# Kernel optimization log

Measured on AMD Instinct MI355X. Metric: run time of the kernel, lower is better.

## Reference

```python
import jax, jax.numpy as jnp
import numpy as np
from jax import lax

WIN_SIZE = 11
SIGMA = 1.5
WEIGHTS = jnp.array([0.0448, 0.2856, 0.3001, 0.2363, 0.1333], dtype=jnp.float32)
C1 = (0.01 * 1.0) ** 2  # val_range = 1.0
C2 = (0.03 * 1.0) ** 2


def gaussian_kernel2d(kernel_size, sigma):
    g = jnp.arange(kernel_size, dtype=jnp.float32) - kernel_size // 2
    g = jnp.exp(-(g ** 2) / (2.0 * sigma ** 2))
    g = g / g.sum()
    return jnp.outer(g, g)  # [k, k]


def depthwise_conv(x, k2d):
    # x: [B, C, H, W]; same gaussian window applied per-channel (groups=C), VALID padding
    C = x.shape[1]
    w = jnp.broadcast_to(k2d, (C, 1) + k2d.shape).astype(x.dtype)
    return lax.conv_general_dilated(x, w, (1, 1), 'VALID',
                                    feature_group_count=C,
                                    dimension_numbers=('NCHW', 'OIHW', 'NCHW'))


def ssim_index(x, y, k2d, nonnegative=True):
    # returns (ss, cs) each of shape [B, C] (spatial mean, per channel)
    m1 = depthwise_conv(x, k2d)
    m2 = depthwise_conv(y, k2d)
    m12 = m1 * m2
    m1s = m1 * m1
    m2s = m2 * m2
    v1 = depthwise_conv(x * x, k2d) - m1s
    v2 = depthwise_conv(y * y, k2d) - m2s
    cov = depthwise_conv(x * y, k2d) - m12
    cs = (2.0 * cov + C2) / (v1 + v2 + C2)
    ss = (2.0 * m12 + C1) / (m1s + m2s + C1) * cs
    ss = ss.reshape(ss.shape[0], ss.shape[1], -1).mean(axis=-1)
    cs = cs.reshape(cs.shape[0], cs.shape[1], -1).mean(axis=-1)
    if nonnegative:
        ss = jnp.maximum(ss, 0.0)
        cs = jnp.maximum(cs, 0.0)
    return ss, cs


def avg_pool2(x):
    # F.avg_pool2d(kernel_size=2). Input spatial dims are even at every scale
    # (512 -> 32), so ceil_mode never pads; plain 2x2/2 mean pooling is exact.
    s = lax.reduce_window(x, jnp.array(0.0, x.dtype), lax.add,
                          (1, 1, 2, 2), (1, 1, 2, 2), 'VALID')
    return s * 0.25


def setup_inputs() -> dict:
    key = jax.random.key(0)
    k1, k2 = jax.random.split(key)
    B, C, H, W = 4, 12, 512, 512
    pred = jax.random.normal(k1, (B, C, H, W), dtype=jnp.float32)
    target = jax.random.randint(k2, (B, H, W), 0, C, dtype=jnp.int64)
    return {"pred": pred, "target": target}


def reference(pred, target):
    # MS_SSIMLoss.forward with process_input=True, nonnegative=True.
    # The per-class python loop in the original is an independent depthwise
    # computation per channel -> vectorized here as a C-channel grouped conv;
    # loss = mean over classes of (1 - mean over batch of msss) == 1 - mean(msss).
    num_classes = pred.shape[1]
    x = jax.nn.softmax(pred, axis=1)
    y = jax.nn.one_hot(target, num_classes, dtype=pred.dtype).transpose(0, 3, 1, 2)
    k2d = gaussian_kernel2d(WIN_SIZE, SIGMA)
    m = WEIGHTS.shape[0]
    vals = []
    for i in range(m):
        if i > 0:
            x = avg_pool2(x)
            y = avg_pool2(y)
        ss, cs = ssim_index(x, y, k2d, nonnegative=True)
        vals.append(cs if i + 1 < m else ss)
    stacked = jnp.stack(vals, axis=-1)  # [B, C, m]
    msss = jnp.prod(stacked ** WEIGHTS, axis=-1)  # [B, C]
    return 1.0 - msss.mean()
```

## Files before the change

kernel.cpp:

```cpp
#include <hip/hip_runtime.h>

#define NCH 12
#define NB  4
#define BC  48
#define HW0 (512 * 512)

#define GK_INIT { 0.00102840f, 0.00759863f, 0.03600078f, 0.10936081f, \
                  0.21300541f, 0.26601164f, 0.21300541f, 0.10936081f, \
                  0.03600078f, 0.00759863f, 0.00102840f }

__global__ __launch_bounds__(256)
void k_prep(const float* __restrict__ pred, const int* __restrict__ tgt,
            float* __restrict__ U, float* __restrict__ X1,
            unsigned short* __restrict__ Y1, double* __restrict__ acc) {
    if (blockIdx.x == 0) {
        for (int t = threadIdx.x; t < 480; t += 256) acc[t] = 0.0;
    }
    const int blk = blockIdx.x;
    const int b  = blk >> 8;
    const int py = blk & 255;
    const int px = threadIdx.x;
    const size_t o00 = (size_t)(2 * py) * 512 + 2 * px;
    const size_t o10 = o00 + 512;
    const float* Pb = pred + (size_t)b * NCH * HW0;

    float ex[NCH], ey[NCH], ez[NCH], ew[NCH];
    float s00 = 0.f, s01 = 0.f, s10 = 0.f, s11 = 0.f;
#pragma unroll
    for (int c = 0; c < NCH; ++c) {
        const float* pc = Pb + (size_t)c * HW0;
        float2 r0 = *(const float2*)(pc + o00);
        float2 r1 = *(const float2*)(pc + o10);
        ex[c] = __expf(r0.x); ey[c] = __expf(r0.y);
        ez[c] = __expf(r1.x); ew[c] = __expf(r1.y);
        s00 += ex[c]; s01 += ey[c]; s10 += ez[c]; s11 += ew[c];
    }
    float u00 = 1.f / s00, u01 = 1.f / s01, u10 = 1.f / s10, u11 = 1.f / s11;
    float* Ub = U + (size_t)b * HW0;
    *(float2*)(Ub + o00) = make_float2(u00, u01);
    *(float2*)(Ub + o10) = make_float2(u10, u11);

    const int* Tb = tgt + (size_t)b * HW0;
    int2 t0 = *(const int2*)(Tb + o00);
    int2 t1 = *(const int2*)(Tb + o10);

#pragma unroll
    for (int c = 0; c < NCH; ++c) {
        float xs = ex[c] * u00 + ey[c] * u01 + ez[c] * u10 + ew[c] * u11;
        size_t oidx = ((size_t)(b * NCH + c) * 256 + py) * 256 + px;
        X1[oidx] = 0.25f * xs;
        unsigned cnt = (unsigned)(t0.x == c) + (unsigned)(t0.y == c)
                     + (unsigned)(t1.x == c) + (unsigned)(t1.y == c);
        Y1[oidx] = (unsigned short)(cnt << 6);
    }
}

union SMem {
    struct {
        float sx[42 * 43 + 4];
        uint2 tm4[42 * 35];
        unsigned long long ybits[30];
        float red[8];
    } s0;
    struct {
        unsigned int sxy[42 * 43 + 4];
        uint2 tm4[42 * 35];
        unsigned short tm5[42 * 35];
        float red[8];
    } rg;
};

__device__ __forceinline__ void ssim0_tile(
    const float* __restrict__ pred, const float* __restrict__ U,
    const int* __restrict__ tgt, double* __restrict__ acc,
    int tile, int bc,
    float* sx, uint2* tm4, unsigned long long* ybits, float* red) {
    constexpr int SS = 43;
    constexpr int TS = 35;
    constexpr int H = 512, W = 512, OH = 502, OW = 502, tilesX = 16;
    const float gk[11] = GK_INIT;

    const int ty = tile / tilesX, tx = tile - ty * tilesX;
    const int oy = ty * 32, ox = tx * 32;
    const int tid = threadIdx.x;
    const bool interior = (oy + 41 < H) && (ox + 41 < W);

    const int b = bc / NCH, cls = bc - (bc / NCH) * NCH;
    const float* Pb = pred + (((size_t)b * NCH + cls) << 18);
    const float* Ub = U + ((size_t)b << 18);
    const int* Tb = tgt + ((size_t)b << 18);

    float pv[7], uv[7];
    int tv[7];
    {
        int r = tid / 42, c = tid - (tid / 42) * 42;
#pragma unroll
        for (int k = 0; k < 7; ++k) {
            bool inr = (k < 6) || (tid < 228);
            int gy = oy + r, gx = ox + c;
            bool ld = inr && (interior || (gy < H && gx < W));
            pv[k] = 0.f; uv[k] = 0.f; tv[k] = -1;
            if (ld) {
                int off = gy * W + gx;
                pv[k] = Pb[off];
                uv[k] = Ub[off];
                tv[k] = Tb[off];
            }
            c += 4; r += 6;
            if (c >= 42) { c -= 42; r += 1; }
        }
    }
    {
        int r = tid / 42, c = tid - (tid / 42) * 42;
#pragma unroll
        for (int k = 0; k < 7; ++k) {
            bool inr = (k < 6) || (tid < 228);
            float xv = __expf(pv[k]) * uv[k];
            bool bit = (tv[k] == cls);
            unsigned long long mk = __ballot(bit);
            if ((tid & 63) == 0) ybits[(tid >> 6) + (k << 2)] = mk;
            if (inr) sx[r * SS + c] = xv;
            c += 4; r += 6;
            if (c >= 42) { c -= 42; r += 1; }
        }
        if (tid == 0) { ybits[28] = 0ull; ybits[29] = 0ull; }
    }
    __syncthreads();

    if (tid < 252) {
        int rr = tid / 6, s = tid - (tid / 6) * 6;
        int c0 = s * 6;
        const float* px = sx + rr * SS + c0;
        float ac0[6] = {}, ac1[6] = {}, ac2[6] = {}, ac3[6] = {};
        unsigned long long win;
        {
            int i0 = rr * 42 + c0;
            int w = i0 >> 6, sh = i0 & 63;
            unsigned long long lo = ybits[w], hi = ybits[w + 1];
            win = sh ? ((lo >> sh) | (hi << (64 - sh))) : lo;
        }
#pragma unroll
        for (int j = 0; j < 16; ++j) {
            float xv = px[j];
            float xx = xv * xv;
            bool bit = (win >> j) & 1;
            float yv = bit ? 1.f : 0.f;
            float xy = bit ? xv : 0.f;
#pragma unroll
            for (int o = 0; o < 6; ++o) {
                int kk = j - o;
                if (kk >= 0 && kk <= 10) {
                    float g = gk[kk];
                    ac0[o] = fmaf(g, xv, ac0[o]);
                    ac1[o] = fmaf(g, yv, ac1[o]);
                    ac2[o] = fmaf(g, xx, ac2[o]);
                    ac3[o] = fmaf(g, xy, ac3[o]);
                }
            }
        }
        int ob = rr * TS + c0;
#pragma unroll
        for (int o = 0; o < 6; ++o) {
            if (c0 + o < 32) {
                unsigned ua = __float_as_uint(ac0[o]);
                unsigned ub = __float_as_uint(ac1[o]);
                unsigned uc = __float_as_uint(ac2[o]);
                unsigned ud = __float_as_uint(ac3[o]);
                tm4[ob + o] = make_uint2((ua >> 16) | (ub & 0xFFFF0000u),
                                         (uc >> 16) | (ud & 0xFFFF0000u));
            }
        }
    }
    __syncthreads();

    const float C1 = 1e-4f, C2 = 9e-4f;
    const int cc = tid & 31, rg = tid >> 5, r0 = rg << 2;
    float a0[4] = {}, a1[4] = {}, a2[4] = {}, a3[4] = {};
    const int vb = r0 * TS + cc;
#pragma unroll
    for (int k = 0; k < 14; ++k) {
        uint2 tv2 = tm4[vb + k * TS];
        float m1v = __uint_as_float(tv2.x << 16);
        float m2v = __uint_as_float(tv2.x & 0xFFFF0000u);
        float xxv = __uint_as_float(tv2.y << 16);
        float xyv = __uint_as_float(tv2.y & 0xFFFF0000u);
#pragma unroll
        for (int j = 0; j < 4; ++j) {
            int kk = k - j;
            if (kk >= 0 && kk <= 10) {
                float g = gk[kk];
                a0[j] = fmaf(g, m1v, a0[j]);
                a1[j] = fmaf(g, m2v, a1[j]);
                a2[j] = fmaf(g, xxv, a2[j]);
                a3[j] = fmaf(g, xyv, a3[j]);
            }
        }
    }
    float cs_l = 0.f, ss_l = 0.f;
    const bool colok = (ox + cc < OW);
#pragma unroll
    for (int j = 0; j < 4; ++j) {
        if (colok && (oy + r0 + j < OH)) {
            float m1 = a0[j], m2 = a1[j];
            float sxx = a2[j], sxy_ = a3[j];
            float m11 = m1 * m1, m22 = m2 * m2, m12 = m1 * m2;
            float v1 = sxx - m11, v2 = m2 - m22, cov = sxy_ - m12;
            float d1 = m11 + m22 + C1, d2 = v1 + v2 + C2;
            float n2 = 2.f * cov + C2;
            float q = 1.f / (d1 * d2);
            cs_l = fmaf(n2 * d1, q, cs_l);
            ss_l = fmaf((2.f * m12 + C1) * n2, q, ss_l);
        }
    }

    for (int off = 32; off; off >>= 1) {
        cs_l += __shfl_down(cs_l, off);
        ss_l += __shfl_down(ss_l, off);
    }
    int wv = tid >> 6, ln = tid & 63;
    if (ln == 0) { red[wv] = cs_l; red[4 + wv] = ss_l; }
    __syncthreads();
    if (tid == 0) {
        double cs_b = (double)red[0] + (double)red[1] + (double)red[2] + (double)red[3];
        double ss_b = (double)red[4] + (double)red[5] + (double)red[6] + (double)red[7];
        atomicAdd(&acc[bc], cs_b);
        atomicAdd(&acc[48 + bc], ss_b);
    }
}

template <int PIN>
__device__ __forceinline__ void ssim_tile_g(
    const float* __restrict__ Xs, const unsigned short* __restrict__ Ys,
    int H, int W, int OH, int OW, int tilesX, int tile, int bc,
    double* __restrict__ acc, int scale,
    unsigned int* sxy, uint2* tm4, unsigned short* tm5, float* red) {
    constexpr int SS = 43;
    constexpr int TS = 35;
    const float gk[11] = GK_INIT;

    const int ty = tile / tilesX, tx = tile - ty * tilesX;
    const int oy = ty * 32, ox = tx * 32;
    const int tid = threadIdx.x;
    const bool interior = (oy + 41 < H) && (ox + 41 < W);

    constexpr int SC = 1 << PIN;
    const int SW = W * SC;
    const float* Xb = Xs + (size_t)bc * H * W * SC * SC;
    const unsigned short* Yb = Ys + (size_t)bc * H * W * SC * SC;

    {
        int r = tid / 42, c = tid - (tid / 42) * 42;
#pragma unroll
        for (int k = 0; k < 7; ++k) {
            bool inr = (k < 6) || (tid < 228);
            int gy = oy + r, gx = ox + c;
            bool ld = inr && (interior || (gy < H && gx < W));
            float xv = 0.f;
            unsigned yc = 0;
            if (ld) {
                if constexpr (PIN == 0) {
                    int off = gy * SW + gx;
                    xv = Xb[off];
                    yc = Yb[off];
                } else {
                    const float* q = Xb + (SC * gy) * SW + SC * gx;
                    const unsigned short* qy = Yb + (SC * gy) * SW + SC * gx;
                    float s = 0.f; unsigned us = 0;
#pragma unroll
                    for (int a = 0; a < SC; ++a) {
                        const float* qr = q + a * SW;
                        const unsigned short* qyr = qy + a * SW;
                        if constexpr (PIN == 1) {
                            float2 f = *(const float2*)qr;
                            s += f.x + f.y;
                            ushort2 uy = *(const ushort2*)qyr;
                            us += (unsigned)uy.x + (unsigned)uy.y;
                        } else {
#pragma unroll
                            for (int e4 = 0; e4 < SC / 4; ++e4) {
                                float4 f = *(const float4*)(qr + e4 * 4);
                                s += (f.x + f.y) + (f.z + f.w);
                                ushort4 uy = *(const ushort4*)(qyr + e4 * 4);
                                us += ((unsigned)uy.x + (unsigned)uy.y)
                                    + ((unsigned)uy.z + (unsigned)uy.w);
                            }
                        }
                    }
                    xv = s * (1.f / (float)(SC * SC));
                    yc = us >> (2 * PIN);
                }
            }
            if (inr) {
                unsigned xb = (__float_as_uint(xv) + 0x8000u) >> 16;
                sxy[r * SS + c] = (yc << 16) | xb;
            }
            c += 4; r += 6;
            if (c >= 42) { c -= 42; r += 1; }
        }
    }
    __syncthreads();

    if (tid < 252) {
        int rr = tid / 6, s = tid - (tid / 6) * 6;
        int c0 = s * 6;
        const unsigned int* pxy = sxy + rr * SS + c0;
        float ac0[6] = {}, ac1[6] = {}, ac2[6] = {}, ac3[6] = {}, ac4[6] = {};
#pragma unroll
        for (int j = 0; j < 16; ++j) {
            unsigned v = pxy[j];
            float xv = __uint_as_float(v << 16);
            float yv = (float)(v >> 16);
            float xx = xv * xv;
            float xy = xv * yv;
            float yy = yv * yv;
#pragma unroll
            for (int o = 0; o < 6; ++o) {
                int kk = j - o;
                if (kk >= 0 && kk <= 10) {
                    float g = gk[kk];
                    ac0[o] = fmaf(g, xv, ac0[o]);
                    ac1[o] = fmaf(g, yv, ac1[o]);
                    ac2[o] = fmaf(g, xx, ac2[o]);
                    ac3[o] = fmaf(g, xy, ac3[o]);
                    ac4[o] = fmaf(g, yy, ac4[o]);
                }
            }
        }
        int ob = rr * TS + c0;
#pragma unroll
        for (int o = 0; o < 6; ++o) {
            if (c0 + o < 32) {
                unsigned ua = __float_as_uint(ac0[o]) + 0x8000u;
                unsigned ub = __float_as_uint(ac1[o]) + 0x8000u;
                unsigned uc = __float_as_uint(ac2[o]) + 0x8000u;
                unsigned ud = __float_as_uint(ac3[o]) + 0x8000u;
                unsigned ue = __float_as_uint(ac4[o]) + 0x8000u;
                tm4[ob + o] = make_uint2((ua >> 16) | (ub & 0xFFFF0000u),
                                         (uc >> 16) | (ud & 0xFFFF0000u));
                tm5[ob + o] = (unsigned short)(ue >> 16);
            }
        }
    }
    __syncthreads();

    const float C1 = 1e-4f, C2 = 9e-4f;
    const int cc = tid & 31, rg = tid >> 5, r0 = rg << 2;
    float a0[4] = {}, a1[4] = {}, a2[4] = {}, a3[4] = {}, a4[4] = {};
    const int vb = r0 * TS + cc;
#pragma unroll
    for (int k = 0; k < 14; ++k) {
        uint2 tv = tm4[vb + k * TS];
        float t0 = __uint_as_float(tv.x << 16);
        float t1 = __uint_as_float(tv.x & 0xFFFF0000u);
        float t2 = __uint_as_float(tv.y << 16);
        float t3 = __uint_as_float(tv.y & 0xFFFF0000u);
        float t4 = __uint_as_float((unsigned)tm5[vb + k * TS] << 16);
#pragma unroll
        for (int j = 0; j < 4; ++j) {
            int kk = k - j;
            if (kk >= 0 && kk <= 10) {
                float g = gk[kk];
                a0[j] = fmaf(g, t0, a0[j]);
                a1[j] = fmaf(g, t1, a1[j]);
                a2[j] = fmaf(g, t2, a2[j]);
                a3[j] = fmaf(g, t3, a3[j]);
                a4[j] = fmaf(g, t4, a4[j]);
            }
        }
    }
    float cs_l = 0.f, ss_l = 0.f;
    const bool colok = (ox + cc < OW);
#pragma unroll
    for (int j = 0; j < 4; ++j) {
        if (colok && (oy + r0 + j < OH)) {
            float m1 = a0[j];
            float m2 = a1[j] * (1.f / 256.f);
            float sxx = a2[j];
            float sxy_ = a3[j] * (1.f / 256.f);
            float syy_ = a4[j] * (1.f / 65536.f);
            float m11 = m1 * m1, m22 = m2 * m2, m12 = m1 * m2;
            float v1 = sxx - m11, v2 = syy_ - m22, cov = sxy_ - m12;
            float d1 = m11 + m22 + C1, d2 = v1 + v2 + C2;
            float n2 = 2.f * cov + C2;
            float q = 1.f / (d1 * d2);
            cs_l = fmaf(n2 * d1, q, cs_l);
            ss_l = fmaf((2.f * m12 + C1) * n2, q, ss_l);
        }
    }

    for (int offs = 32; offs; offs >>= 1) {
        cs_l += __shfl_down(cs_l, offs);
        ss_l += __shfl_down(ss_l, offs);
    }
    int wv = tid >> 6, ln = tid & 63;
    if (ln == 0) { red[wv] = cs_l; red[4 + wv] = ss_l; }
    __syncthreads();
    if (tid == 0) {
        double cs_b = (double)red[0] + (double)red[1] + (double)red[2] + (double)red[3];
        double ss_b = (double)red[4] + (double)red[5] + (double)red[6] + (double)red[7];
        atomicAdd(&acc[scale * 96 + bc], cs_b);
        atomicAdd(&acc[scale * 96 + 48 + bc], ss_b);
    }
}

__global__ __launch_bounds__(256, 7)
void k_main(const float* __restrict__ pred, const float* __restrict__ U,
            const int* __restrict__ tgt,
            const float* __restrict__ X1, const unsigned short* __restrict__ Y1,
            double* __restrict__ acc) {
    __shared__ SMem sm;
    const int gb = blockIdx.x;

    int s0_idx = -1, rest_idx = -1;
    if (gb < 16320) {
        int r = gb & 3, q = gb >> 2;
        if (r == 0) rest_idx = q;
        else        s0_idx = 3 * q + (r - 1);
    } else {
        s0_idx = 12240 + (gb - 16320);
    }

    if (s0_idx >= 0) {
        ssim0_tile(pred, U, tgt, acc, s0_idx & 255, s0_idx >> 8,
                   sm.s0.sx, sm.s0.tm4, sm.s0.ybits, sm.s0.red);
        return;
    }
    const int gq = rest_idx;
    if (gq < 48) {
        ssim_tile_g<3>(X1, Y1, 32, 32, 22, 22, 1, 0, gq,
                       acc, 4, sm.rg.sxy, sm.rg.tm4, sm.rg.tm5, sm.rg.red);
    } else if (gq < 240) {
        int t = gq - 48;
        ssim_tile_g<2>(X1, Y1, 64, 64, 54, 54, 2, t & 3, t >> 2,
                       acc, 3, sm.rg.sxy, sm.rg.tm4, sm.rg.tm5, sm.rg.red);
    } else if (gq < 1008) {
        int t = gq - 240;
        ssim_tile_g<1>(X1, Y1, 128, 128, 118, 118, 4, t & 15, t >> 4,
                       acc, 2, sm.rg.sxy, sm.rg.tm4, sm.rg.tm5, sm.rg.red);
    } else {
        int t = gq - 1008;
        ssim_tile_g<0>(X1, Y1, 256, 256, 246, 246, 8, t & 63, t >> 6,
                       acc, 1, sm.rg.sxy, sm.rg.tm4, sm.rg.tm5, sm.rg.red);
    }
}

__global__ void k_final(const double* __restrict__ acc, float* __restrict__ out) {
    const float wts[5] = {0.0448f, 0.2856f, 0.3001f, 0.2363f, 0.1333f};
    const float cnt[5] = {252004.f, 60516.f, 13924.f, 2916.f, 484.f};
    int tid = threadIdx.x;
    float msss = 0.f;
    if (tid < BC) {
        msss = 1.f;
#pragma unroll
        for (int s = 0; s < 5; ++s) {
            double a = (s < 4) ? acc[s * 96 + tid] : acc[s * 96 + 48 + tid];
            float v = fmaxf((float)(a / (double)cnt[s]), 0.f);
            msss *= powf(v, wts[s]);
        }
    }
    for (int off = 32; off; off >>= 1) msss += __shfl_down(msss, off);
    if (tid == 0) out[0] = 1.f - msss * (1.f / (float)BC);
}

extern "C" void kernel_launch(void* const* d_in, const int* in_sizes, int n_in,
                              void* d_out, int out_size, void* d_ws, size_t ws_size,
                              hipStream_t stream) {
    const float* pred = (const float*)d_in[0];
    const int*   tgt  = (const int*)d_in[1];
    float* out = (float*)d_out;

    double* acc = (double*)d_ws;
    float* U  = (float*)(acc + 480);
    float* X1 = U + (size_t)NB * HW0;
    unsigned short* Y1 = (unsigned short*)(X1 + (size_t)BC * 65536);

    k_prep<<<1024, 256, 0, stream>>>(pred, tgt, U, X1, Y1, acc);

    k_main<<<16368, 256, 0, stream>>>(pred, U, tgt, X1, Y1, acc);

    k_final<<<1, 64, 0, stream>>>(acc, out);
}
```

Before: 213.8 us.

## Pack softmax reciprocal with target one-hot bits and interleave bf16 x with y counts

The prep kernel now writes one 32-bit word per pixel that holds the softmax reciprocal rounded to bf16 in the high half and a one-hot class bitmask in the low bits. The scale-0 tiles therefore read two arrays instead of three, and no longer read the int target. The half-resolution pooled x (bf16) and y count are also interleaved into a single 32-bit array, so the coarse scales issue one load stream instead of two. This is meant to cut global memory traffic and load instructions, at the cost of lower precision for the reciprocal at scale 0 and for the pooled inputs before the later poolings.

```diff
diff --git a/kernel.cpp b/kernel.cpp
--- a/kernel.cpp
+++ b/kernel.cpp
@@ -11,8 +11,8 @@
 
 __global__ __launch_bounds__(256)
 void k_prep(const float* __restrict__ pred, const int* __restrict__ tgt,
-            float* __restrict__ U, float* __restrict__ X1,
-            unsigned short* __restrict__ Y1, double* __restrict__ acc) {
+            unsigned* __restrict__ UT, unsigned* __restrict__ XY1,
+            double* __restrict__ acc) {
     if (blockIdx.x == 0) {
         for (int t = threadIdx.x; t < 480; t += 256) acc[t] = 0.0;
     }
@@ -36,22 +36,29 @@
         s00 += ex[c]; s01 += ey[c]; s10 += ez[c]; s11 += ew[c];
     }
     float u00 = 1.f / s00, u01 = 1.f / s01, u10 = 1.f / s10, u11 = 1.f / s11;
-    float* Ub = U + (size_t)b * HW0;
-    *(float2*)(Ub + o00) = make_float2(u00, u01);
-    *(float2*)(Ub + o10) = make_float2(u10, u11);
 
     const int* Tb = tgt + (size_t)b * HW0;
     int2 t0 = *(const int2*)(Tb + o00);
     int2 t1 = *(const int2*)(Tb + o10);
 
+    unsigned* UTb = UT + (size_t)b * HW0;
+    {
+        unsigned w00 = (((__float_as_uint(u00) + 0x8000u) >> 16) << 16) | (1u << t0.x);
+        unsigned w01 = (((__float_as_uint(u01) + 0x8000u) >> 16) << 16) | (1u << t0.y);
+        unsigned w10 = (((__float_as_uint(u10) + 0x8000u) >> 16) << 16) | (1u << t1.x);
+        unsigned w11 = (((__float_as_uint(u11) + 0x8000u) >> 16) << 16) | (1u << t1.y);
+        *(uint2*)(UTb + o00) = make_uint2(w00, w01);
+        *(uint2*)(UTb + o10) = make_uint2(w10, w11);
+    }
+
 #pragma unroll
     for (int c = 0; c < NCH; ++c) {
-        float xs = ex[c] * u00 + ey[c] * u01 + ez[c] * u10 + ew[c] * u11;
-        size_t oidx = ((size_t)(b * NCH + c) * 256 + py) * 256 + px;
-        X1[oidx] = 0.25f * xs;
+        float xs = 0.25f * (ex[c] * u00 + ey[c] * u01 + ez[c] * u10 + ew[c] * u11);
+        unsigned xb = (__float_as_uint(xs) + 0x8000u) >> 16;
         unsigned cnt = (unsigned)(t0.x == c) + (unsigned)(t0.y == c)
                      + (unsigned)(t1.x == c) + (unsigned)(t1.y == c);
-        Y1[oidx] = (unsigned short)(cnt << 6);
+        size_t oidx = ((size_t)(b * NCH + c) * 256 + py) * 256 + px;
+        XY1[oidx] = ((cnt << 6) << 16) | xb;
     }
 }
 
@@ -71,9 +78,8 @@
 };
 
 __device__ __forceinline__ void ssim0_tile(
-    const float* __restrict__ pred, const float* __restrict__ U,
-    const int* __restrict__ tgt, double* __restrict__ acc,
-    int tile, int bc,
+    const float* __restrict__ pred, const unsigned* __restrict__ UT,
+    double* __restrict__ acc, int tile, int bc,
     float* sx, uint2* tm4, unsigned long long* ybits, float* red) {
     constexpr int SS = 43;
     constexpr int TS = 35;
@@ -87,11 +93,10 @@
 
     const int b = bc / NCH, cls = bc - (bc / NCH) * NCH;
     const float* Pb = pred + (((size_t)b * NCH + cls) << 18);
-    const float* Ub = U + ((size_t)b << 18);
-    const int* Tb = tgt + ((size_t)b << 18);
-
-    float pv[7], uv[7];
-    int tv[7];
+    const unsigned* Ub = UT + ((size_t)b << 18);
+
+    float pv[7];
+    unsigned uw[7];
     {
         int r = tid / 42, c = tid - (tid / 42) * 42;
 #pragma unroll
@@ -99,12 +104,11 @@
             bool inr = (k < 6) || (tid < 228);
             int gy = oy + r, gx = ox + c;
             bool ld = inr && (interior || (gy < H && gx < W));
-            pv[k] = 0.f; uv[k] = 0.f; tv[k] = -1;
+            pv[k] = 0.f; uw[k] = 0u;
             if (ld) {
                 int off = gy * W + gx;
                 pv[k] = Pb[off];
-                uv[k] = Ub[off];
-                tv[k] = Tb[off];
+                uw[k] = Ub[off];
             }
             c += 4; r += 6;
             if (c >= 42) { c -= 42; r += 1; }
@@ -115,8 +119,9 @@
 #pragma unroll
         for (int k = 0; k < 7; ++k) {
             bool inr = (k < 6) || (tid < 228);
-            float xv = __expf(pv[k]) * uv[k];
-            bool bit = (tv[k] == cls);
+            float uf = __uint_as_float(uw[k] & 0xFFFF0000u);
+            float xv = __expf(pv[k]) * uf;
+            bool bit = (uw[k] >> cls) & 1;
             unsigned long long mk = __ballot(bit);
             if ((tid & 63) == 0) ybits[(tid >> 6) + (k << 2)] = mk;
             if (inr) sx[r * SS + c] = xv;
@@ -230,7 +235,7 @@
 
 template <int PIN>
 __device__ __forceinline__ void ssim_tile_g(
-    const float* __restrict__ Xs, const unsigned short* __restrict__ Ys,
+    const unsigned* __restrict__ XYs,
     int H, int W, int OH, int OW, int tilesX, int tile, int bc,
     double* __restrict__ acc, int scale,
     unsigned int* sxy, uint2* tm4, unsigned short* tm5, float* red) {
@@ -245,8 +250,7 @@
 
     constexpr int SC = 1 << PIN;
     const int SW = W * SC;
-    const float* Xb = Xs + (size_t)bc * H * W * SC * SC;
-    const unsigned short* Yb = Ys + (size_t)bc * H * W * SC * SC;
+    const unsigned* Xb = XYs + (size_t)bc * H * W * SC * SC;
 
     {
         int r = tid / 42, c = tid - (tid / 42) * 42;
@@ -255,45 +259,41 @@
             bool inr = (k < 6) || (tid < 228);
             int gy = oy + r, gx = ox + c;
             bool ld = inr && (interior || (gy < H && gx < W));
-            float xv = 0.f;
-            unsigned yc = 0;
+            unsigned wout = 0u;
             if (ld) {
                 if constexpr (PIN == 0) {
-                    int off = gy * SW + gx;
-                    xv = Xb[off];
-                    yc = Yb[off];
+                    wout = Xb[gy * SW + gx];
                 } else {
-                    const float* q = Xb + (SC * gy) * SW + SC * gx;
-                    const unsigned short* qy = Yb + (SC * gy) * SW + SC * gx;
+                    const unsigned* q = Xb + (SC * gy) * SW + SC * gx;
                     float s = 0.f; unsigned us = 0;
 #pragma unroll
                     for (int a = 0; a < SC; ++a) {
-                        const float* qr = q + a * SW;
-                        const unsigned short* qyr = qy + a * SW;
+                        const unsigned* qr = q + a * SW;
                         if constexpr (PIN == 1) {
-                            float2 f = *(const float2*)qr;
-                            s += f.x + f.y;
-                            ushort2 uy = *(const ushort2*)qyr;
-                            us += (unsigned)uy.x + (unsigned)uy.y;
+                            uint2 w2 = *(const uint2*)qr;
+                            s += __uint_as_float(w2.x << 16)
+                               + __uint_as_float(w2.y << 16);
+                            us += (w2.x >> 16) + (w2.y >> 16);
                         } else {
 #pragma unroll
                             for (int e4 = 0; e4 < SC / 4; ++e4) {
-                                float4 f = *(const float4*)(qr + e4 * 4);
-                                s += (f.x + f.y) + (f.z + f.w);
-                                ushort4 uy = *(const ushort4*)(qyr + e4 * 4);
-                                us += ((unsigned)uy.x + (unsigned)uy.y)
-                                    + ((unsigned)uy.z + (unsigned)uy.w);
+                                uint4 w4 = *(const uint4*)(qr + e4 * 4);
+                                s += (__uint_as_float(w4.x << 16)
+                                    + __uint_as_float(w4.y << 16))
+                                   + (__uint_as_float(w4.z << 16)
+                                    + __uint_as_float(w4.w << 16));
+                                us += ((w4.x >> 16) + (w4.y >> 16))
+                                    + ((w4.z >> 16) + (w4.w >> 16));
                             }
                         }
                     }
-                    xv = s * (1.f / (float)(SC * SC));
-                    yc = us >> (2 * PIN);
+                    float xv = s * (1.f / (float)(SC * SC));
+                    unsigned yc = us >> (2 * PIN);
+                    unsigned xb = (__float_as_uint(xv) + 0x8000u) >> 16;
+                    wout = (yc << 16) | xb;
                 }
             }
-            if (inr) {
-                unsigned xb = (__float_as_uint(xv) + 0x8000u) >> 16;
-                sxy[r * SS + c] = (yc << 16) | xb;
-            }
+            if (inr) sxy[r * SS + c] = wout;
             c += 4; r += 6;
             if (c >= 42) { c -= 42; r += 1; }
         }
@@ -404,10 +404,8 @@
 }
 
 __global__ __launch_bounds__(256, 7)
-void k_main(const float* __restrict__ pred, const float* __restrict__ U,
-            const int* __restrict__ tgt,
-            const float* __restrict__ X1, const unsigned short* __restrict__ Y1,
-            double* __restrict__ acc) {
+void k_main(const float* __restrict__ pred, const unsigned* __restrict__ UT,
+            const unsigned* __restrict__ XY1, double* __restrict__ acc) {
     __shared__ SMem sm;
     const int gb = blockIdx.x;
 
@@ -421,25 +419,25 @@
     }
 
     if (s0_idx >= 0) {
-        ssim0_tile(pred, U, tgt, acc, s0_idx & 255, s0_idx >> 8,
+        ssim0_tile(pred, UT, acc, s0_idx & 255, s0_idx >> 8,
                    sm.s0.sx, sm.s0.tm4, sm.s0.ybits, sm.s0.red);
         return;
     }
     const int gq = rest_idx;
     if (gq < 48) {
-        ssim_tile_g<3>(X1, Y1, 32, 32, 22, 22, 1, 0, gq,
+        ssim_tile_g<3>(XY1, 32, 32, 22, 22, 1, 0, gq,
                        acc, 4, sm.rg.sxy, sm.rg.tm4, sm.rg.tm5, sm.rg.red);
     } else if (gq < 240) {
         int t = gq - 48;
-        ssim_tile_g<2>(X1, Y1, 64, 64, 54, 54, 2, t & 3, t >> 2,
+        ssim_tile_g<2>(XY1, 64, 64, 54, 54, 2, t & 3, t >> 2,
                        acc, 3, sm.rg.sxy, sm.rg.tm4, sm.rg.tm5, sm.rg.red);
     } else if (gq < 1008) {
         int t = gq - 240;
-        ssim_tile_g<1>(X1, Y1, 128, 128, 118, 118, 4, t & 15, t >> 4,
+        ssim_tile_g<1>(XY1, 128, 128, 118, 118, 4, t & 15, t >> 4,
                        acc, 2, sm.rg.sxy, sm.rg.tm4, sm.rg.tm5, sm.rg.red);
     } else {
         int t = gq - 1008;
-        ssim_tile_g<0>(X1, Y1, 256, 256, 246, 246, 8, t & 63, t >> 6,
+        ssim_tile_g<0>(XY1, 256, 256, 246, 246, 8, t & 63, t >> 6,
                        acc, 1, sm.rg.sxy, sm.rg.tm4, sm.rg.tm5, sm.rg.red);
     }
 }
@@ -470,13 +468,12 @@
     float* out = (float*)d_out;
 
     double* acc = (double*)d_ws;
-    float* U  = (float*)(acc + 480);
-    float* X1 = U + (size_t)NB * HW0;
-    unsigned short* Y1 = (unsigned short*)(X1 + (size_t)BC * 65536);
-
-    k_prep<<<1024, 256, 0, stream>>>(pred, tgt, U, X1, Y1, acc);
-
-    k_main<<<16368, 256, 0, stream>>>(pred, U, tgt, X1, Y1, acc);
+    unsigned* UT  = (unsigned*)(acc + 480);
+    unsigned* XY1 = UT + (size_t)NB * HW0;
+
+    k_prep<<<1024, 256, 0, stream>>>(pred, tgt, UT, XY1, acc);
+
+    k_main<<<16368, 256, 0, stream>>>(pred, UT, XY1, acc);
 
     k_final<<<1, 64, 0, stream>>>(acc, out);
 }
```

Result: no change. 211.2 us, median of 2 (-1.2%).
